# Optimization experiments

Hardware: AMD Instinct MI355X
Metric: run time of the kernel (lower is better)

Reference implementation:

```python
import jax, jax.numpy as jnp
import numpy as np

N, D, E, OUT = 100000, 128, 600000, 128


def setup_inputs() -> dict:
    key = jax.random.key(0)
    k1, k2, k3, k4, k5 = jax.random.split(key, 5)
    x = jax.random.normal(k1, (N, D), dtype=jnp.float32)
    # Linear params (stored as [in, out]; y = h @ W + b, same math as nn.Linear)
    W = jax.random.normal(k2, (D, OUT), dtype=jnp.float32) * (1.0 / np.sqrt(D))
    b = jax.random.normal(k3, (OUT,), dtype=jnp.float32) * 0.01
    # Flattened ragged neighbor lists as COO edges: node edge_dst[e] aggregates x[edge_src[e]]
    edge_src = jax.random.randint(k4, (E,), 0, N, dtype=jnp.int32)
    edge_dst = jnp.sort(jax.random.randint(k5, (E,), 0, N, dtype=jnp.int32))
    return {"x": x, "W": W, "b": b, "edge_src": edge_src, "edge_dst": edge_dst}


def reference(x, W, b, edge_src, edge_dst):
    n = x.shape[0]
    # segment-mean of neighbor features per destination node
    neigh_sum = jax.ops.segment_sum(x[edge_src], edge_dst, num_segments=n)  # [N, D]
    deg = jax.ops.segment_sum(jnp.ones((edge_dst.shape[0],), x.dtype), edge_dst, num_segments=n)  # [N]
    # nodes with no neighbors keep zero mean (matches `if neigh:` branch)
    neigh_mean = neigh_sum / jnp.maximum(deg, 1.0)[:, None]
    h = x + neigh_mean
    return jax.nn.relu(h @ W + b)
```

## Files before the change

### kernel.cpp

```cpp
#include <hip/hip_runtime.h>
#include <hip/hip_bf16.h>


#define FD  128
#define BR  64
#define HSB 136

typedef __attribute__((ext_vector_type(8))) short bf16x8;
typedef __attribute__((ext_vector_type(4))) float f32x4;

__device__ __forceinline__ short f2bf(float f) {
    unsigned u = __float_as_uint(f);
    return (short)((u + 0x7FFFu + ((u >> 16) & 1u)) >> 16);
}
__device__ __forceinline__ float bf2f(short s) {
    return __uint_as_float(((unsigned)(unsigned short)s) << 16);
}

__global__ __launch_bounds__(256) void prep_full_kernel(
    const float* __restrict__ x, const float* __restrict__ W,
    const int* __restrict__ edst, int* __restrict__ rp,
    short* __restrict__ pkW, short* __restrict__ xb, int N, int E)
{
    const int gid = blockIdx.x * 256 + threadIdx.x;
    const int nth = gridDim.x * 256;

    const int nv = N * FD / 8;
    for (int i = gid; i < nv; i += nth) {
        float4 f0 = *(const float4*)(x + (size_t)i * 8);
        float4 f1 = *(const float4*)(x + (size_t)i * 8 + 4);
        short tmp[8] = {f2bf(f0.x), f2bf(f0.y), f2bf(f0.z), f2bf(f0.w),
                        f2bf(f1.x), f2bf(f1.y), f2bf(f1.z), f2bf(f1.w)};
        *(bf16x8*)(xb + (size_t)i * 8) = *(bf16x8*)tmp;
    }
    for (int e = gid; e < E; e += nth) {
        int cur = edst[e];
        int prev = e ? edst[e - 1] : -1;
        for (int v = prev + 1; v <= cur; ++v) rp[v] = e;
        if (e == E - 1)
            for (int v = cur + 1; v <= N; ++v) rp[v] = E;
    }
    if (gid < 2048) {
        int wave = gid >> 9, rem = gid & 511;
        int ct = rem >> 8, rem2 = rem & 255;
        int kt = rem2 >> 6, lane = rem2 & 63;
        int q = lane >> 4, lr = lane & 15;
        int col = wave * 32 + ct * 16 + lr;
        int k0 = kt * 32 + q * 8;
        short tmp[8];
#pragma unroll
        for (int e2 = 0; e2 < 8; ++e2)
            tmp[e2] = f2bf(W[(size_t)(k0 + e2) * FD + col]);
        *(bf16x8*)(pkW + (size_t)gid * 8) = *(bf16x8*)tmp;
    }
}

__global__ __launch_bounds__(256) void meanagg_main2_kernel(
    const short* __restrict__ xb, const short* __restrict__ pkW,
    const float* __restrict__ bias, const int* __restrict__ esrc,
    const int* __restrict__ rp, float* __restrict__ out, int N, int E)
{
    __shared__ short shb[BR * HSB];
    __shared__ int seg[BR + 1];

    const int t = threadIdx.x;
    const int base = blockIdx.x * BR;

    if (t < BR + 1) {
        int idx = base + t;
        seg[t] = rp[idx > N ? N : idx];
    }
    __syncthreads();

    const int wave = t >> 6;
    const int lane = t & 63;
    const int qw = lane >> 4;
    const int ql = lane & 15;
    const int qb = qw << 4;
    const int rowbase = wave * 16;

    {
        int rb0 = rowbase + qw;
        int r0  = base + rb0;
        int s = (r0 < N) ? seg[rb0] : 0;
        int e = (r0 < N) ? seg[rb0 + 1] : 0;
        int srcv_n = (s + ql < e) ? esrc[s + ql] : 0;
        bf16x8 xv_n = {0, 0, 0, 0, 0, 0, 0, 0};
        if (r0 < N) xv_n = *(const bf16x8*)(xb + (size_t)r0 * FD + 8 * ql);

        for (int it = 0; it < 4; ++it) {
            const int cur_rb = rowbase + it * 4 + qw;
            const int cur_r  = base + cur_rb;
            const int cs0 = s, ce = e;
            int srcv = srcv_n;
            const bf16x8 xv = xv_n;

            if (it < 3) {
                int nrb = rowbase + (it + 1) * 4 + qw;
                int nr  = base + nrb;
                s = (nr < N) ? seg[nrb] : 0;
                e = (nr < N) ? seg[nrb + 1] : 0;
                srcv_n = (s + ql < e) ? esrc[s + ql] : 0;
                bf16x8 z = {0, 0, 0, 0, 0, 0, 0, 0};
                xv_n = z;
                if (nr < N) xv_n = *(const bf16x8*)(xb + (size_t)nr * FD + 8 * ql);
            }

            if (cur_r < N) {
                float a[8];
#pragma unroll
                for (int p = 0; p < 8; ++p) a[p] = 0.f;

                for (int cs = cs0; cs < ce; cs += 16) {
                    int m = ce - cs; if (m > 16) m = 16;
                    if (cs != cs0)
                        srcv = (cs + ql < ce) ? esrc[cs + ql] : 0;
                    for (int j0 = 0; j0 < m; j0 += 6) {
                        uint4 v[6];
#pragma unroll
                        for (int u = 0; u < 6; ++u) {
                            int jj = j0 + u;
                            int idx = __shfl(srcv, qb + (jj & 15));
                            if (jj >= m) idx = 0;
                            v[u] = *(const uint4*)(xb + (size_t)idx * FD + 8 * ql);
                        }
#pragma unroll
                        for (int u = 0; u < 6; ++u) {
                            float f = (j0 + u < m) ? 1.f : 0.f;
                            unsigned w;
                            w = v[u].x;
                            a[0] = fmaf(__uint_as_float(w << 16), f, a[0]);
                            a[1] = fmaf(__uint_as_float(w & 0xFFFF0000u), f, a[1]);
                            w = v[u].y;
                            a[2] = fmaf(__uint_as_float(w << 16), f, a[2]);
                            a[3] = fmaf(__uint_as_float(w & 0xFFFF0000u), f, a[3]);
                            w = v[u].z;
                            a[4] = fmaf(__uint_as_float(w << 16), f, a[4]);
                            a[5] = fmaf(__uint_as_float(w & 0xFFFF0000u), f, a[5]);
                            w = v[u].w;
                            a[6] = fmaf(__uint_as_float(w << 16), f, a[6]);
                            a[7] = fmaf(__uint_as_float(w & 0xFFFF0000u), f, a[7]);
                        }
                    }
                }
                int deg = ce - cs0;
                float inv = 1.0f / (float)(deg > 0 ? deg : 1);
                short hb[8];
#pragma unroll
                for (int p = 0; p < 8; ++p)
                    hb[p] = f2bf(bf2f(xv[p]) + a[p] * inv);
                *(bf16x8*)(shb + cur_rb * HSB + 8 * ql) = *(bf16x8*)hb;
            }
        }
    }
    __syncthreads();

    const int lr = lane & 15;
    const int q  = lane >> 4;
    const int colb = wave * 32;

    bf16x8 bfr[2][4];
#pragma unroll
    for (int ct = 0; ct < 2; ++ct)
#pragma unroll
        for (int kt = 0; kt < 4; ++kt) {
            int f = ((wave * 2 + ct) * 4 + kt) * 64 + lane;
            bfr[ct][kt] = *(const bf16x8*)(pkW + (size_t)f * 8);
        }

    f32x4 acc[4][2];
#pragma unroll
    for (int rt = 0; rt < 4; ++rt) {
        acc[rt][0] = (f32x4){0.f, 0.f, 0.f, 0.f};
        acc[rt][1] = (f32x4){0.f, 0.f, 0.f, 0.f};
    }

#pragma unroll
    for (int rt = 0; rt < 4; ++rt)
#pragma unroll
        for (int kt = 0; kt < 4; ++kt) {
            bf16x8 av = *(const bf16x8*)(shb + (rt * 16 + lr) * HSB + kt * 32 + q * 8);
            acc[rt][0] = __builtin_amdgcn_mfma_f32_16x16x32_bf16(av, bfr[0][kt], acc[rt][0], 0, 0, 0);
            acc[rt][1] = __builtin_amdgcn_mfma_f32_16x16x32_bf16(av, bfr[1][kt], acc[rt][1], 0, 0, 0);
        }

    const float b0 = bias[colb + lr];
    const float b1 = bias[colb + 16 + lr];

#pragma unroll
    for (int rt = 0; rt < 4; ++rt)
#pragma unroll
        for (int j = 0; j < 4; ++j) {
            int row = base + rt * 16 + q * 4 + j;
            if (row < N) {
                float v0 = acc[rt][0][j] + b0; v0 = v0 > 0.f ? v0 : 0.f;
                float v1 = acc[rt][1][j] + b1; v1 = v1 > 0.f ? v1 : 0.f;
                out[(size_t)row * FD + colb + lr]      = v0;
                out[(size_t)row * FD + colb + 16 + lr] = v1;
            }
        }
}

__global__ __launch_bounds__(256) void prep_kernel(
    const float* __restrict__ W, const int* __restrict__ edst,
    int* __restrict__ rp, short* __restrict__ pkW, int N, int E)
{
    int gid = blockIdx.x * 256 + threadIdx.x;
    if (gid < E) {
        int cur = edst[gid];
        int prev = gid ? edst[gid - 1] : -1;
        for (int v = prev + 1; v <= cur; ++v) rp[v] = gid;
        if (gid == E - 1)
            for (int v = cur + 1; v <= N; ++v) rp[v] = E;
    }
    if (gid < 2048) {
        int wave = gid >> 9, rem = gid & 511;
        int ct = rem >> 8, rem2 = rem & 255;
        int kt = rem2 >> 6, lane = rem2 & 63;
        int q = lane >> 4, lr = lane & 15;
        int col = wave * 32 + ct * 16 + lr;
        int k0 = kt * 32 + q * 8;
        short tmp[8];
#pragma unroll
        for (int e = 0; e < 8; ++e)
            tmp[e] = f2bf(W[(size_t)(k0 + e) * FD + col]);
        *(bf16x8*)(pkW + (size_t)gid * 8) = *(bf16x8*)tmp;
    }
}

__global__ __launch_bounds__(256) void meanagg_main_kernel(
    const float* __restrict__ x, const short* __restrict__ pkW,
    const float* __restrict__ bias, const int* __restrict__ esrc,
    const int* __restrict__ rp, float* __restrict__ out, int N, int E)
{
    __shared__ short shb[BR * HSB];
    __shared__ int seg[BR + 1];

    const int t = threadIdx.x;
    const int base = blockIdx.x * BR;

    if (t < BR + 1) {
        int idx = base + t;
        seg[t] = rp[idx > N ? N : idx];
    }
    __syncthreads();

    const int wave = t >> 6;
    const int lane = t & 63;
    const int sw = lane >> 5;
    const int sl = lane & 31;
    const int lb = sw << 5;
    const int rowbase = wave * 16;

    {
        int rb0 = rowbase + sw;
        int r0  = base + rb0;
        int s0  = (r0 < N) ? seg[rb0] : 0;
        int e0  = (r0 < N) ? seg[rb0 + 1] : 0;
        int src_next = (s0 + sl < e0) ? esrc[s0 + sl] : 0;
        float4 xv_next = make_float4(0.f, 0.f, 0.f, 0.f);
        if (r0 < N) xv_next = *(const float4*)(x + (size_t)r0 * FD + 4 * sl);

        int s = s0, e = e0;
        for (int it = 0; it < 8; ++it) {
            const int cur_rb = rowbase + it * 2 + sw;
            const int cur_r  = base + cur_rb;
            const int cur_s  = s, cur_e = e;
            const int src_l  = src_next;
            const float4 xv  = xv_next;

            if (it < 7) {
                int nrb = rowbase + (it + 1) * 2 + sw;
                int nr  = base + nrb;
                s = (nr < N) ? seg[nrb] : 0;
                e = (nr < N) ? seg[nrb + 1] : 0;
                src_next = (s + sl < e) ? esrc[s + sl] : 0;
                xv_next = make_float4(0.f, 0.f, 0.f, 0.f);
                if (nr < N) xv_next = *(const float4*)(x + (size_t)nr * FD + 4 * sl);
            }

            if (cur_r < N) {
                float4 a0 = make_float4(0.f, 0.f, 0.f, 0.f), a1 = a0;
                int srcv = src_l;
                for (int cs = cur_s; cs < cur_e; cs += 32) {
                    int m = cur_e - cs; if (m > 32) m = 32;
                    if (cs != cur_s)
                        srcv = (cs + sl < cur_e) ? esrc[cs + sl] : 0;
                    for (int j0 = 0; j0 < m; j0 += 8) {
                        const int rem = m - j0;
                        float4 v[8];
#pragma unroll
                        for (int u = 0; u < 8; ++u) {
                            int idx = __shfl(srcv, lb + ((j0 + u) & 31));
                            v[u] = *(const float4*)(x + (size_t)idx * FD + 4 * sl);
                        }
#pragma unroll
                        for (int u = 0; u < 8; ++u) {
                            float f = (u < rem) ? 1.f : 0.f;
                            float4* A = (u & 1) ? &a1 : &a0;
                            A->x = fmaf(v[u].x, f, A->x);
                            A->y = fmaf(v[u].y, f, A->y);
                            A->z = fmaf(v[u].z, f, A->z);
                            A->w = fmaf(v[u].w, f, A->w);
                        }
                    }
                }
                int deg = cur_e - cur_s;
                float inv = 1.0f / (float)(deg > 0 ? deg : 1);
                short4 hb;
                hb.x = f2bf(xv.x + (a0.x + a1.x) * inv);
                hb.y = f2bf(xv.y + (a0.y + a1.y) * inv);
                hb.z = f2bf(xv.z + (a0.z + a1.z) * inv);
                hb.w = f2bf(xv.w + (a0.w + a1.w) * inv);
                *(short4*)(shb + cur_rb * HSB + 4 * sl) = hb;
            }
        }
    }
    __syncthreads();

    const int lr = lane & 15;
    const int q  = lane >> 4;
    const int colb = wave * 32;

    bf16x8 bfr[2][4];
#pragma unroll
    for (int ct = 0; ct < 2; ++ct)
#pragma unroll
        for (int kt = 0; kt < 4; ++kt) {
            int f = ((wave * 2 + ct) * 4 + kt) * 64 + lane;
            bfr[ct][kt] = *(const bf16x8*)(pkW + (size_t)f * 8);
        }

    f32x4 acc[4][2];
#pragma unroll
    for (int rt = 0; rt < 4; ++rt) {
        acc[rt][0] = (f32x4){0.f, 0.f, 0.f, 0.f};
        acc[rt][1] = (f32x4){0.f, 0.f, 0.f, 0.f};
    }

#pragma unroll
    for (int rt = 0; rt < 4; ++rt)
#pragma unroll
        for (int kt = 0; kt < 4; ++kt) {
            bf16x8 av = *(const bf16x8*)(shb + (rt * 16 + lr) * HSB + kt * 32 + q * 8);
            acc[rt][0] = __builtin_amdgcn_mfma_f32_16x16x32_bf16(av, bfr[0][kt], acc[rt][0], 0, 0, 0);
            acc[rt][1] = __builtin_amdgcn_mfma_f32_16x16x32_bf16(av, bfr[1][kt], acc[rt][1], 0, 0, 0);
        }

    const float b0 = bias[colb + lr];
    const float b1 = bias[colb + 16 + lr];

#pragma unroll
    for (int rt = 0; rt < 4; ++rt)
#pragma unroll
        for (int j = 0; j < 4; ++j) {
            int row = base + rt * 16 + q * 4 + j;
            if (row < N) {
                float v0 = acc[rt][0][j] + b0; v0 = v0 > 0.f ? v0 : 0.f;
                float v1 = acc[rt][1][j] + b1; v1 = v1 > 0.f ? v1 : 0.f;
                out[(size_t)row * FD + colb + lr]      = v0;
                out[(size_t)row * FD + colb + 16 + lr] = v1;
            }
        }
}

__global__ __launch_bounds__(256) void meanagg_fused_kernel(
    const float* __restrict__ x, const float* __restrict__ W,
    const float* __restrict__ bias, const int* __restrict__ esrc,
    const int* __restrict__ edst, float* __restrict__ out, int N, int E)
{
    __shared__ short shb[BR * HSB];
    __shared__ int seg[BR + 1];

    const int t = threadIdx.x;
    const int base = blockIdx.x * BR;

    if (t < BR + 1) {
        int v = base + t;
        int lo = 0, hi = E;
        while (lo < hi) {
            int mid = (lo + hi) >> 1;
            if (edst[mid] < v) lo = mid + 1; else hi = mid;
        }
        seg[t] = lo;
    }
    __syncthreads();

    const int wave = t >> 6;
    const int lane = t & 63;
    const int sw = lane >> 5;
    const int sl = lane & 31;
    const int lb = sw << 5;
    const int rowbase = wave * 16;

    for (int it = 0; it < 8; ++it) {
        int cur_rb = rowbase + it * 2 + sw;
        int cur_r  = base + cur_rb;
        if (cur_r >= N) break;
        int cur_s = seg[cur_rb], cur_e = seg[cur_rb + 1];
        float4 a0 = make_float4(0.f, 0.f, 0.f, 0.f), a1 = a0;
        for (int cs = cur_s; cs < cur_e; cs += 32) {
            int m = cur_e - cs; if (m > 32) m = 32;
            int srcv = (cs + sl < cur_e) ? esrc[cs + sl] : 0;
            for (int j0 = 0; j0 < m; j0 += 8) {
                const int rem = m - j0;
#pragma unroll
                for (int u = 0; u < 8; ++u) {
                    int idx = __shfl(srcv, lb + ((j0 + u) & 31));
                    float4 v = *(const float4*)(x + (size_t)idx * FD + 4 * sl);
                    float f = (u < rem) ? 1.f : 0.f;
                    float4* A = (u & 1) ? &a1 : &a0;
                    A->x = fmaf(v.x, f, A->x);
                    A->y = fmaf(v.y, f, A->y);
                    A->z = fmaf(v.z, f, A->z);
                    A->w = fmaf(v.w, f, A->w);
                }
            }
        }
        float4 xv = *(const float4*)(x + (size_t)cur_r * FD + 4 * sl);
        int deg = cur_e - cur_s;
        float inv = 1.0f / (float)(deg > 0 ? deg : 1);
        short4 hb;
        hb.x = f2bf(xv.x + (a0.x + a1.x) * inv);
        hb.y = f2bf(xv.y + (a0.y + a1.y) * inv);
        hb.z = f2bf(xv.z + (a0.z + a1.z) * inv);
        hb.w = f2bf(xv.w + (a0.w + a1.w) * inv);
        *(short4*)(shb + cur_rb * HSB + 4 * sl) = hb;
    }
    __syncthreads();

    const int lr = lane & 15;
    const int q  = lane >> 4;
    const int colb = wave * 32;

    bf16x8 bfr[2][4];
#pragma unroll
    for (int ct = 0; ct < 2; ++ct) {
        int col = colb + ct * 16 + lr;
#pragma unroll
        for (int kt = 0; kt < 4; ++kt) {
            bf16x8 f;
#pragma unroll
            for (int e = 0; e < 8; ++e)
                f[e] = f2bf(W[(size_t)(kt * 32 + q * 8 + e) * FD + col]);
            bfr[ct][kt] = f;
        }
    }

    f32x4 acc[4][2];
#pragma unroll
    for (int rt = 0; rt < 4; ++rt) {
        acc[rt][0] = (f32x4){0.f, 0.f, 0.f, 0.f};
        acc[rt][1] = (f32x4){0.f, 0.f, 0.f, 0.f};
    }

#pragma unroll
    for (int rt = 0; rt < 4; ++rt)
#pragma unroll
        for (int kt = 0; kt < 4; ++kt) {
            bf16x8 av = *(const bf16x8*)(shb + (rt * 16 + lr) * HSB + kt * 32 + q * 8);
            acc[rt][0] = __builtin_amdgcn_mfma_f32_16x16x32_bf16(av, bfr[0][kt], acc[rt][0], 0, 0, 0);
            acc[rt][1] = __builtin_amdgcn_mfma_f32_16x16x32_bf16(av, bfr[1][kt], acc[rt][1], 0, 0, 0);
        }

    const float b0 = bias[colb + lr];
    const float b1 = bias[colb + 16 + lr];

#pragma unroll
    for (int rt = 0; rt < 4; ++rt)
#pragma unroll
        for (int j = 0; j < 4; ++j) {
            int row = base + rt * 16 + q * 4 + j;
            if (row < N) {
                float v0 = acc[rt][0][j] + b0; v0 = v0 > 0.f ? v0 : 0.f;
                float v1 = acc[rt][1][j] + b1; v1 = v1 > 0.f ? v1 : 0.f;
                out[(size_t)row * FD + colb + lr]      = v0;
                out[(size_t)row * FD + colb + 16 + lr] = v1;
            }
        }
}

extern "C" void kernel_launch(void* const* d_in, const int* in_sizes, int n_in,
                              void* d_out, int out_size, void* d_ws, size_t ws_size,
                              hipStream_t stream) {
    const float* x    = (const float*)d_in[0];
    const float* W    = (const float*)d_in[1];
    const float* bias = (const float*)d_in[2];
    const int* esrc   = (const int*)d_in[3];
    const int* edst   = (const int*)d_in[4];
    float* out        = (float*)d_out;

    int N = in_sizes[0] / FD;
    int E = in_sizes[3];
    int blocks = (N + BR - 1) / BR;

    size_t rp_bytes = (size_t)(N + 1) * 4;
    size_t pk_off   = (rp_bytes + 511) & ~(size_t)511;
    size_t xb_off   = (pk_off + 2048 * 8 * 2 + 511) & ~(size_t)511;
    size_t need_med = pk_off + 2048 * 8 * 2;
    size_t need_big = xb_off + (size_t)N * FD * 2;

    if (ws_size >= need_big) {
        int* rp    = (int*)d_ws;
        short* pkW = (short*)((char*)d_ws + pk_off);
        short* xb  = (short*)((char*)d_ws + xb_off);
        prep_full_kernel<<<2048, 256, 0, stream>>>(x, W, edst, rp, pkW, xb, N, E);
        meanagg_main2_kernel<<<blocks, 256, 0, stream>>>(xb, pkW, bias, esrc, rp, out, N, E);
    } else if (ws_size >= need_med) {
        int* rp    = (int*)d_ws;
        short* pkW = (short*)((char*)d_ws + pk_off);
        int pblocks = (E + 255) / 256;
        prep_kernel<<<pblocks, 256, 0, stream>>>(W, edst, rp, pkW, N, E);
        meanagg_main_kernel<<<blocks, 256, 0, stream>>>(x, pkW, bias, esrc, rp, out, N, E);
    } else {
        meanagg_fused_kernel<<<blocks, 256, 0, stream>>>(x, W, bias, esrc, edst, out, N, E);
    }
}
```

Baseline: 57.65 us.

## Gather neighbor features from an FP8 copy of x in a new aggregation kernel

The prep kernel now also writes an FP8 (e4m3) copy of x plus a zero sentinel row. A new main kernel gathers neighbor rows from this 1-byte-per-element copy, so each gather moves half the bytes of the bf16 path. Each lane handles 16 features, and all 8 neighbor loads for two rows are issued up front, with a tail loop for higher degrees. The self term still reads bf16, but the neighbor sum loses precision through FP8 quantization, and the prep kernel now writes an extra buffer.

After: 61.91 us. 7.4% more time.

```diff
diff --git a/kernel.cpp b/kernel.cpp
--- a/kernel.cpp
+++ b/kernel.cpp
@@ -8,6 +8,7 @@
 
 typedef __attribute__((ext_vector_type(8))) short bf16x8;
 typedef __attribute__((ext_vector_type(4))) float f32x4;
+typedef __attribute__((ext_vector_type(2))) float f32x2;
 
 __device__ __forceinline__ short f2bf(float f) {
     unsigned u = __float_as_uint(f);
@@ -17,10 +18,73 @@
     return __uint_as_float(((unsigned)(unsigned short)s) << 16);
 }
 
+#if __has_builtin(__builtin_amdgcn_cvt_pk_f32_fp8) && __has_builtin(__builtin_amdgcn_cvt_pk_fp8_f32)
+#define FP8_HW 1
+#else
+#define FP8_HW 0
+#endif
+
+#if !FP8_HW
+__device__ __forceinline__ float fp8_to_f(unsigned b) {
+    unsigned s = (b >> 7) & 1, e = (b >> 3) & 15, m = b & 7;
+    float v = (e == 0) ? ldexpf((float)m, -9) : ldexpf((float)(m + 8), (int)e - 10);
+    return s ? -v : v;
+}
+__device__ __forceinline__ unsigned f_to_fp8(float f) {
+    unsigned u = __float_as_uint(f);
+    unsigned s = u >> 31;
+    u &= 0x7fffffffu;
+    if (u > 0x43e00000u) u = 0x43e00000u;
+    float af = __uint_as_float(u);
+    unsigned bits;
+    if (af < 7.62939453125e-06f) bits = 0;
+    else {
+        int e; float m = frexpf(af, &e);
+        if (e < -5) {
+            int mi = (int)(af * 512.f + 0.5f);
+            bits = (mi > 7) ? 0x08u : (unsigned)mi;
+        } else {
+            int mi = (int)(m * 16.f + 0.5f);
+            int E = e + 6;
+            if (mi == 16) { mi = 8; E += 1; }
+            if (E > 15) { E = 15; mi = 14; }
+            if (E == 15 && mi == 15) mi = 14;
+            bits = ((unsigned)E << 3) | (unsigned)(mi - 8);
+        }
+    }
+    return bits | (s << 7);
+}
+#endif
+
+__device__ __forceinline__ f32x2 fp8lo(unsigned w) {
+#if FP8_HW
+    return __builtin_amdgcn_cvt_pk_f32_fp8(w, false);
+#else
+    f32x2 r; r.x = fp8_to_f(w & 0xffu); r.y = fp8_to_f((w >> 8) & 0xffu); return r;
+#endif
+}
+__device__ __forceinline__ f32x2 fp8hi(unsigned w) {
+#if FP8_HW
+    return __builtin_amdgcn_cvt_pk_f32_fp8(w, true);
+#else
+    f32x2 r; r.x = fp8_to_f((w >> 16) & 0xffu); r.y = fp8_to_f((w >> 24) & 0xffu); return r;
+#endif
+}
+__device__ __forceinline__ unsigned fp8pack4(float a, float b, float c, float d) {
+#if FP8_HW
+    int w = __builtin_amdgcn_cvt_pk_fp8_f32(a, b, 0, false);
+    w = __builtin_amdgcn_cvt_pk_fp8_f32(c, d, w, true);
+    return (unsigned)w;
+#else
+    return f_to_fp8(a) | (f_to_fp8(b) << 8) | (f_to_fp8(c) << 16) | (f_to_fp8(d) << 24);
+#endif
+}
+
 __global__ __launch_bounds__(256) void prep_full_kernel(
     const float* __restrict__ x, const float* __restrict__ W,
     const int* __restrict__ edst, int* __restrict__ rp,
-    short* __restrict__ pkW, short* __restrict__ xb, int N, int E)
+    short* __restrict__ pkW, short* __restrict__ xb,
+    unsigned char* __restrict__ xq, int do_q, int N, int E)
 {
     const int gid = blockIdx.x * 256 + threadIdx.x;
     const int nth = gridDim.x * 256;
@@ -32,6 +96,17 @@
         short tmp[8] = {f2bf(f0.x), f2bf(f0.y), f2bf(f0.z), f2bf(f0.w),
                         f2bf(f1.x), f2bf(f1.y), f2bf(f1.z), f2bf(f1.w)};
         *(bf16x8*)(xb + (size_t)i * 8) = *(bf16x8*)tmp;
+        if (do_q) {
+            uint2 q;
+            q.x = fp8pack4(f0.x, f0.y, f0.z, f0.w);
+            q.y = fp8pack4(f1.x, f1.y, f1.z, f1.w);
+            *(uint2*)(xq + (size_t)i * 8) = q;
+        }
+    }
+    if (gid < 16) {
+        bf16x8 z = {0, 0, 0, 0, 0, 0, 0, 0};
+        *(bf16x8*)(xb + (size_t)N * FD + gid * 8) = z;
+        if (do_q) *(uint2*)(xq + (size_t)N * FD + gid * 8) = make_uint2(0u, 0u);
     }
     for (int e = gid; e < E; e += nth) {
         int cur = edst[e];
@@ -40,12 +115,14 @@
         if (e == E - 1)
             for (int v = cur + 1; v <= N; ++v) rp[v] = E;
     }
+    if (E == 0)
+        for (int v = gid; v <= N; v += nth) rp[v] = 0;
     if (gid < 2048) {
-        int wave = gid >> 9, rem = gid & 511;
+        int wv = gid >> 9, rem = gid & 511;
         int ct = rem >> 8, rem2 = rem & 255;
         int kt = rem2 >> 6, lane = rem2 & 63;
         int q = lane >> 4, lr = lane & 15;
-        int col = wave * 32 + ct * 16 + lr;
+        int col = wv * 32 + ct * 16 + lr;
         int k0 = kt * 32 + q * 8;
         short tmp[8];
 #pragma unroll
@@ -53,6 +130,190 @@
             tmp[e2] = f2bf(W[(size_t)(k0 + e2) * FD + col]);
         *(bf16x8*)(pkW + (size_t)gid * 8) = *(bf16x8*)tmp;
     }
+}
+
+__device__ __forceinline__ void issue8q(const unsigned char* __restrict__ xq, int srcv,
+                                        int ob, int ol, int m, int N, uint4 v[8])
+{
+#pragma unroll
+    for (int u = 0; u < 8; ++u) {
+        int idx = __shfl(srcv, ob + u);
+        if (u >= m) idx = N;
+        v[u] = *(const uint4*)(xq + (size_t)idx * FD + 16 * ol);
+    }
+}
+
+__device__ __forceinline__ void acc8q(const uint4 v[8], f32x2 a[8])
+{
+#pragma unroll
+    for (int u = 0; u < 8; ++u) {
+        a[0] += fp8lo(v[u].x); a[1] += fp8hi(v[u].x);
+        a[2] += fp8lo(v[u].y); a[3] += fp8hi(v[u].y);
+        a[4] += fp8lo(v[u].z); a[5] += fp8hi(v[u].z);
+        a[6] += fp8lo(v[u].w); a[7] += fp8hi(v[u].w);
+    }
+}
+
+__device__ __forceinline__ void issue4q(const unsigned char* __restrict__ xq, int srcv,
+                                        int ob, int ol, int j0, int m, int N, uint4 v[4])
+{
+#pragma unroll
+    for (int u = 0; u < 4; ++u) {
+        int jj = j0 + u;
+        int idx = __shfl(srcv, ob + (jj & 7));
+        if (jj >= m) idx = N;
+        v[u] = *(const uint4*)(xq + (size_t)idx * FD + 16 * ol);
+    }
+}
+
+__device__ __forceinline__ void acc4q(const uint4 v[4], f32x2 a[8])
+{
+#pragma unroll
+    for (int u = 0; u < 4; ++u) {
+        a[0] += fp8lo(v[u].x); a[1] += fp8hi(v[u].x);
+        a[2] += fp8lo(v[u].y); a[3] += fp8hi(v[u].y);
+        a[4] += fp8lo(v[u].z); a[5] += fp8hi(v[u].z);
+        a[6] += fp8lo(v[u].w); a[7] += fp8hi(v[u].w);
+    }
+}
+
+__device__ void tailq(const unsigned char* __restrict__ xq, const int* __restrict__ esrc,
+                      int s, int e, int ob, int ol, int N, int E, f32x2 a[8])
+{
+    if (e - s <= 8) return;
+    uint4 v2[4];
+    for (int cs = s + 8; cs < e; cs += 8) {
+        int ad = cs + ol; if (ad > E - 1) ad = E - 1; if (ad < 0) ad = 0;
+        int sv = esrc[ad];
+        int m = e - cs; if (m > 8) m = 8;
+        issue4q(xq, sv, ob, ol, 0, m, N, v2); acc4q(v2, a);
+        issue4q(xq, sv, ob, ol, 4, m, N, v2); acc4q(v2, a);
+    }
+}
+
+__device__ __forceinline__ void finq(short* shb, int rb, int ol,
+                                     const bf16x8 xva, const bf16x8 xvb,
+                                     const f32x2 a[8], int deg)
+{
+    float inv = 1.0f / (float)(deg > 0 ? deg : 1);
+    short hb[16];
+#pragma unroll
+    for (int j = 0; j < 8; ++j) {
+        short xlo = (j < 4) ? xva[2 * j]     : xvb[2 * (j - 4)];
+        short xhi = (j < 4) ? xva[2 * j + 1] : xvb[2 * (j - 4) + 1];
+        hb[2 * j]     = f2bf(bf2f(xlo) + a[j].x * inv);
+        hb[2 * j + 1] = f2bf(bf2f(xhi) + a[j].y * inv);
+    }
+    *(bf16x8*)(shb + rb * HSB + 16 * ol)     = *(bf16x8*)hb;
+    *(bf16x8*)(shb + rb * HSB + 16 * ol + 8) = *(bf16x8*)(hb + 8);
+}
+
+__global__ __launch_bounds__(256) void meanagg_main5_kernel(
+    const short* __restrict__ xb, const unsigned char* __restrict__ xq,
+    const short* __restrict__ pkW, const float* __restrict__ bias,
+    const int* __restrict__ esrc, const int* __restrict__ rp,
+    float* __restrict__ out, int N, int E)
+{
+    __shared__ short shb[BR * HSB];
+    __shared__ int seg[BR + 1];
+
+    const int t = threadIdx.x;
+    const int base = blockIdx.x * BR;
+
+    if (t < BR + 1) {
+        int idx = base + t;
+        seg[t] = rp[idx > N ? N : idx];
+    }
+    __syncthreads();
+
+    const int wave = t >> 6;
+    const int lane = t & 63;
+    const int oc = lane >> 3;
+    const int ol = lane & 7;
+    const int ob = oc << 3;
+
+    const int rb0 = wave * 16 + oc;
+    const int rb1 = rb0 + 8;
+    const int r0c = (base + rb0 > N) ? N : base + rb0;
+    const int r1c = (base + rb1 > N) ? N : base + rb1;
+
+    const int s0 = seg[rb0], e0 = seg[rb0 + 1];
+    const int s1 = seg[rb1], e1 = seg[rb1 + 1];
+    const int d0 = e0 - s0, d1 = e1 - s1;
+
+    int ad0 = s0 + ol; if (ad0 > E - 1) ad0 = E - 1; if (ad0 < 0) ad0 = 0;
+    int ad1 = s1 + ol; if (ad1 > E - 1) ad1 = E - 1; if (ad1 < 0) ad1 = 0;
+    const int srcv0 = esrc[ad0];
+    const int srcv1 = esrc[ad1];
+
+    const bf16x8 xv0a = *(const bf16x8*)(xb + (size_t)r0c * FD + 16 * ol);
+    const bf16x8 xv0b = *(const bf16x8*)(xb + (size_t)r0c * FD + 16 * ol + 8);
+    const bf16x8 xv1a = *(const bf16x8*)(xb + (size_t)r1c * FD + 16 * ol);
+    const bf16x8 xv1b = *(const bf16x8*)(xb + (size_t)r1c * FD + 16 * ol + 8);
+
+    uint4 v0[8], v1[8];
+    issue8q(xq, srcv0, ob, ol, d0 < 8 ? d0 : 8, N, v0);
+    issue8q(xq, srcv1, ob, ol, d1 < 8 ? d1 : 8, N, v1);
+
+    f32x2 a[8];
+#pragma unroll
+    for (int p = 0; p < 8; ++p) a[p] = (f32x2){0.f, 0.f};
+    acc8q(v0, a);
+    tailq(xq, esrc, s0, e0, ob, ol, N, E, a);
+    finq(shb, rb0, ol, xv0a, xv0b, a, d0);
+
+#pragma unroll
+    for (int p = 0; p < 8; ++p) a[p] = (f32x2){0.f, 0.f};
+    acc8q(v1, a);
+    tailq(xq, esrc, s1, e1, ob, ol, N, E, a);
+    finq(shb, rb1, ol, xv1a, xv1b, a, d1);
+
+    __syncthreads();
+
+    const int lr = lane & 15;
+    const int q  = lane >> 4;
+    const int colb = wave * 32;
+
+    bf16x8 bfr[2][4];
+#pragma unroll
+    for (int ct = 0; ct < 2; ++ct)
+#pragma unroll
+        for (int kt = 0; kt < 4; ++kt) {
+            int f = ((wave * 2 + ct) * 4 + kt) * 64 + lane;
+            bfr[ct][kt] = *(const bf16x8*)(pkW + (size_t)f * 8);
+        }
+
+    f32x4 acc[4][2];
+#pragma unroll
+    for (int rt = 0; rt < 4; ++rt) {
+        acc[rt][0] = (f32x4){0.f, 0.f, 0.f, 0.f};
+        acc[rt][1] = (f32x4){0.f, 0.f, 0.f, 0.f};
+    }
+
+#pragma unroll
+    for (int rt = 0; rt < 4; ++rt)
+#pragma unroll
+        for (int kt = 0; kt < 4; ++kt) {
+            bf16x8 av = *(const bf16x8*)(shb + (rt * 16 + lr) * HSB + kt * 32 + q * 8);
+            acc[rt][0] = __builtin_amdgcn_mfma_f32_16x16x32_bf16(av, bfr[0][kt], acc[rt][0], 0, 0, 0);
+            acc[rt][1] = __builtin_amdgcn_mfma_f32_16x16x32_bf16(av, bfr[1][kt], acc[rt][1], 0, 0, 0);
+        }
+
+    const float b0 = bias[colb + lr];
+    const float b1 = bias[colb + 16 + lr];
+
+#pragma unroll
+    for (int rt = 0; rt < 4; ++rt)
+#pragma unroll
+        for (int j = 0; j < 4; ++j) {
+            int row = base + rt * 16 + q * 4 + j;
+            if (row < N) {
+                float o0 = acc[rt][0][j] + b0; o0 = o0 > 0.f ? o0 : 0.f;
+                float o1 = acc[rt][1][j] + b1; o1 = o1 > 0.f ? o1 : 0.f;
+                out[(size_t)row * FD + colb + lr]      = o0;
+                out[(size_t)row * FD + colb + 16 + lr] = o1;
+            }
+        }
 }
 
 __global__ __launch_bounds__(256) void meanagg_main2_kernel(
@@ -107,9 +368,9 @@
             }
 
             if (cur_r < N) {
-                float a[8];
-#pragma unroll
-                for (int p = 0; p < 8; ++p) a[p] = 0.f;
+                float av[8];
+#pragma unroll
+                for (int p = 0; p < 8; ++p) av[p] = 0.f;
 
                 for (int cs = cs0; cs < ce; cs += 16) {
                     int m = ce - cs; if (m > 16) m = 16;
@@ -129,17 +390,17 @@
                             float f = (j0 + u < m) ? 1.f : 0.f;
                             unsigned w;
                             w = v[u].x;
-                            a[0] = fmaf(__uint_as_float(w << 16), f, a[0]);
-                            a[1] = fmaf(__uint_as_float(w & 0xFFFF0000u), f, a[1]);
+                            av[0] = fmaf(__uint_as_float(w << 16), f, av[0]);
+                            av[1] = fmaf(__uint_as_float(w & 0xFFFF0000u), f, av[1]);
                             w = v[u].y;
-                            a[2] = fmaf(__uint_as_float(w << 16), f, a[2]);
-                            a[3] = fmaf(__uint_as_float(w & 0xFFFF0000u), f, a[3]);
+                            av[2] = fmaf(__uint_as_float(w << 16), f, av[2]);
+                            av[3] = fmaf(__uint_as_float(w & 0xFFFF0000u), f, av[3]);
                             w = v[u].z;
-                            a[4] = fmaf(__uint_as_float(w << 16), f, a[4]);
-                            a[5] = fmaf(__uint_as_float(w & 0xFFFF0000u), f, a[5]);
+                            av[4] = fmaf(__uint_as_float(w << 16), f, av[4]);
+                            av[5] = fmaf(__uint_as_float(w & 0xFFFF0000u), f, av[5]);
                             w = v[u].w;
-                            a[6] = fmaf(__uint_as_float(w << 16), f, a[6]);
-                            a[7] = fmaf(__uint_as_float(w & 0xFFFF0000u), f, a[7]);
+                            av[6] = fmaf(__uint_as_float(w << 16), f, av[6]);
+                            av[7] = fmaf(__uint_as_float(w & 0xFFFF0000u), f, av[7]);
                         }
                     }
                 }
@@ -148,171 +409,8 @@
                 short hb[8];
 #pragma unroll
                 for (int p = 0; p < 8; ++p)
-                    hb[p] = f2bf(bf2f(xv[p]) + a[p] * inv);
+                    hb[p] = f2bf(bf2f(xv[p]) + av[p] * inv);
                 *(bf16x8*)(shb + cur_rb * HSB + 8 * ql) = *(bf16x8*)hb;
-            }
-        }
-    }
-    __syncthreads();
-
-    const int lr = lane & 15;
-    const int q  = lane >> 4;
-    const int colb = wave * 32;
-
-    bf16x8 bfr[2][4];
-#pragma unroll
-    for (int ct = 0; ct < 2; ++ct)
-#pragma unroll
-        for (int kt = 0; kt < 4; ++kt) {
-            int f = ((wave * 2 + ct) * 4 + kt) * 64 + lane;
-            bfr[ct][kt] = *(const bf16x8*)(pkW + (size_t)f * 8);
-        }
-
-    f32x4 acc[4][2];
-#pragma unroll
-    for (int rt = 0; rt < 4; ++rt) {
-        acc[rt][0] = (f32x4){0.f, 0.f, 0.f, 0.f};
-        acc[rt][1] = (f32x4){0.f, 0.f, 0.f, 0.f};
-    }
-
-#pragma unroll
-    for (int rt = 0; rt < 4; ++rt)
-#pragma unroll
-        for (int kt = 0; kt < 4; ++kt) {
-            bf16x8 av = *(const bf16x8*)(shb + (rt * 16 + lr) * HSB + kt * 32 + q * 8);
-            acc[rt][0] = __builtin_amdgcn_mfma_f32_16x16x32_bf16(av, bfr[0][kt], acc[rt][0], 0, 0, 0);
-            acc[rt][1] = __builtin_amdgcn_mfma_f32_16x16x32_bf16(av, bfr[1][kt], acc[rt][1], 0, 0, 0);
-        }
-
-    const float b0 = bias[colb + lr];
-    const float b1 = bias[colb + 16 + lr];
-
-#pragma unroll
-    for (int rt = 0; rt < 4; ++rt)
-#pragma unroll
-        for (int j = 0; j < 4; ++j) {
-            int row = base + rt * 16 + q * 4 + j;
-            if (row < N) {
-                float v0 = acc[rt][0][j] + b0; v0 = v0 > 0.f ? v0 : 0.f;
-                float v1 = acc[rt][1][j] + b1; v1 = v1 > 0.f ? v1 : 0.f;
-                out[(size_t)row * FD + colb + lr]      = v0;
-                out[(size_t)row * FD + colb + 16 + lr] = v1;
-            }
-        }
-}
-
-__global__ __launch_bounds__(256) void prep_kernel(
-    const float* __restrict__ W, const int* __restrict__ edst,
-    int* __restrict__ rp, short* __restrict__ pkW, int N, int E)
-{
-    int gid = blockIdx.x * 256 + threadIdx.x;
-    if (gid < E) {
-        int cur = edst[gid];
-        int prev = gid ? edst[gid - 1] : -1;
-        for (int v = prev + 1; v <= cur; ++v) rp[v] = gid;
-        if (gid == E - 1)
-            for (int v = cur + 1; v <= N; ++v) rp[v] = E;
-    }
-    if (gid < 2048) {
-        int wave = gid >> 9, rem = gid & 511;
-        int ct = rem >> 8, rem2 = rem & 255;
-        int kt = rem2 >> 6, lane = rem2 & 63;
-        int q = lane >> 4, lr = lane & 15;
-        int col = wave * 32 + ct * 16 + lr;
-        int k0 = kt * 32 + q * 8;
-        short tmp[8];
-#pragma unroll
-        for (int e = 0; e < 8; ++e)
-            tmp[e] = f2bf(W[(size_t)(k0 + e) * FD + col]);
-        *(bf16x8*)(pkW + (size_t)gid * 8) = *(bf16x8*)tmp;
-    }
-}
-
-__global__ __launch_bounds__(256) void meanagg_main_kernel(
-    const float* __restrict__ x, const short* __restrict__ pkW,
-    const float* __restrict__ bias, const int* __restrict__ esrc,
-    const int* __restrict__ rp, float* __restrict__ out, int N, int E)
-{
-    __shared__ short shb[BR * HSB];
-    __shared__ int seg[BR + 1];
-
-    const int t = threadIdx.x;
-    const int base = blockIdx.x * BR;
-
-    if (t < BR + 1) {
-        int idx = base + t;
-        seg[t] = rp[idx > N ? N : idx];
-    }
-    __syncthreads();
-
-    const int wave = t >> 6;
-    const int lane = t & 63;
-    const int sw = lane >> 5;
-    const int sl = lane & 31;
-    const int lb = sw << 5;
-    const int rowbase = wave * 16;
-
-    {
-        int rb0 = rowbase + sw;
-        int r0  = base + rb0;
-        int s0  = (r0 < N) ? seg[rb0] : 0;
-        int e0  = (r0 < N) ? seg[rb0 + 1] : 0;
-        int src_next = (s0 + sl < e0) ? esrc[s0 + sl] : 0;
-        float4 xv_next = make_float4(0.f, 0.f, 0.f, 0.f);
-        if (r0 < N) xv_next = *(const float4*)(x + (size_t)r0 * FD + 4 * sl);
-
-        int s = s0, e = e0;
-        for (int it = 0; it < 8; ++it) {
-            const int cur_rb = rowbase + it * 2 + sw;
-            const int cur_r  = base + cur_rb;
-            const int cur_s  = s, cur_e = e;
-            const int src_l  = src_next;
-            const float4 xv  = xv_next;
-
-            if (it < 7) {
-                int nrb = rowbase + (it + 1) * 2 + sw;
-                int nr  = base + nrb;
-                s = (nr < N) ? seg[nrb] : 0;
-                e = (nr < N) ? seg[nrb + 1] : 0;
-                src_next = (s + sl < e) ? esrc[s + sl] : 0;
-                xv_next = make_float4(0.f, 0.f, 0.f, 0.f);
-                if (nr < N) xv_next = *(const float4*)(x + (size_t)nr * FD + 4 * sl);
-            }
-
-            if (cur_r < N) {
-                float4 a0 = make_float4(0.f, 0.f, 0.f, 0.f), a1 = a0;
-                int srcv = src_l;
-                for (int cs = cur_s; cs < cur_e; cs += 32) {
-                    int m = cur_e - cs; if (m > 32) m = 32;
-                    if (cs != cur_s)
-                        srcv = (cs + sl < cur_e) ? esrc[cs + sl] : 0;
-                    for (int j0 = 0; j0 < m; j0 += 8) {
-                        const int rem = m - j0;
-                        float4 v[8];
-#pragma unroll
-                        for (int u = 0; u < 8; ++u) {
-                            int idx = __shfl(srcv, lb + ((j0 + u) & 31));
-                            v[u] = *(const float4*)(x + (size_t)idx * FD + 4 * sl);
-                        }
-#pragma unroll
-                        for (int u = 0; u < 8; ++u) {
-                            float f = (u < rem) ? 1.f : 0.f;
-                            float4* A = (u & 1) ? &a1 : &a0;
-                            A->x = fmaf(v[u].x, f, A->x);
-                            A->y = fmaf(v[u].y, f, A->y);
-                            A->z = fmaf(v[u].z, f, A->z);
-                            A->w = fmaf(v[u].w, f, A->w);
-                        }
-                    }
-                }
-                int deg = cur_e - cur_s;
-                float inv = 1.0f / (float)(deg > 0 ? deg : 1);
-                short4 hb;
-                hb.x = f2bf(xv.x + (a0.x + a1.x) * inv);
-                hb.y = f2bf(xv.y + (a0.y + a1.y) * inv);
-                hb.z = f2bf(xv.z + (a0.z + a1.z) * inv);
-                hb.w = f2bf(xv.w + (a0.w + a1.w) * inv);
-                *(short4*)(shb + cur_rb * HSB + 4 * sl) = hb;
             }
         }
     }
@@ -417,14 +515,14 @@
                 }
             }
         }
-        float4 xv = *(const float4*)(x + (size_t)cur_r * FD + 4 * sl);
+        float4 xvv = *(const float4*)(x + (size_t)cur_r * FD + 4 * sl);
         int deg = cur_e - cur_s;
         float inv = 1.0f / (float)(deg > 0 ? deg : 1);
         short4 hb;
-        hb.x = f2bf(xv.x + (a0.x + a1.x) * inv);
-        hb.y = f2bf(xv.y + (a0.y + a1.y) * inv);
-        hb.z = f2bf(xv.z + (a0.z + a1.z) * inv);
-        hb.w = f2bf(xv.w + (a0.w + a1.w) * inv);
+        hb.x = f2bf(xvv.x + (a0.x + a1.x) * inv);
+        hb.y = f2bf(xvv.y + (a0.y + a1.y) * inv);
+        hb.z = f2bf(xvv.z + (a0.z + a1.z) * inv);
+        hb.w = f2bf(xvv.w + (a0.w + a1.w) * inv);
         *(short4*)(shb + cur_rb * HSB + 4 * sl) = hb;
     }
     __syncthreads();
@@ -497,21 +595,23 @@
     size_t rp_bytes = (size_t)(N + 1) * 4;
     size_t pk_off   = (rp_bytes + 511) & ~(size_t)511;
     size_t xb_off   = (pk_off + 2048 * 8 * 2 + 511) & ~(size_t)511;
-    size_t need_med = pk_off + 2048 * 8 * 2;
-    size_t need_big = xb_off + (size_t)N * FD * 2;
-
-    if (ws_size >= need_big) {
+    size_t xq_off   = (xb_off + (size_t)(N + 1) * FD * 2 + 511) & ~(size_t)511;
+    size_t need_t1  = xb_off + (size_t)(N + 1) * FD * 2;
+    size_t need_t0  = xq_off + (size_t)(N + 1) * FD;
+
+    if (ws_size >= need_t0) {
         int* rp    = (int*)d_ws;
         short* pkW = (short*)((char*)d_ws + pk_off);
         short* xb  = (short*)((char*)d_ws + xb_off);
-        prep_full_kernel<<<2048, 256, 0, stream>>>(x, W, edst, rp, pkW, xb, N, E);
-        meanagg_main2_kernel<<<blocks, 256, 0, stream>>>(xb, pkW, bias, esrc, rp, out, N, E);
-    } else if (ws_size >= need_med) {
+        unsigned char* xq = (unsigned char*)((char*)d_ws + xq_off);
+        prep_full_kernel<<<2048, 256, 0, stream>>>(x, W, edst, rp, pkW, xb, xq, 1, N, E);
+        meanagg_main5_kernel<<<blocks, 256, 0, stream>>>(xb, xq, pkW, bias, esrc, rp, out, N, E);
+    } else if (ws_size >= need_t1) {
         int* rp    = (int*)d_ws;
         short* pkW = (short*)((char*)d_ws + pk_off);
-        int pblocks = (E + 255) / 256;
-        prep_kernel<<<pblocks, 256, 0, stream>>>(W, edst, rp, pkW, N, E);
-        meanagg_main_kernel<<<blocks, 256, 0, stream>>>(x, pkW, bias, esrc, rp, out, N, E);
+        short* xb  = (short*)((char*)d_ws + xb_off);
+        prep_full_kernel<<<2048, 256, 0, stream>>>(x, W, edst, rp, pkW, xb, (unsigned char*)xb, 0, N, E);
+        meanagg_main2_kernel<<<blocks, 256, 0, stream>>>(xb, pkW, bias, esrc, rp, out, N, E);
     } else {
         meanagg_fused_kernel<<<blocks, 256, 0, stream>>>(x, W, bias, esrc, edst, out, N, E);
     }
```
